# Kernel tuning notes

Hardware: AMD Instinct MI355X
Metric: run time of the kernel (lower is better)

The kernel has to match this reference:

```python
import jax, jax.numpy as jnp
import numpy as np
from jax import lax

S = 2048      # seq_len
E = 512       # loc_emb_size
H = 512       # hidden_size
V = 50000     # loc_size
WIN = 11      # window: j in [i-10, i]
LAMBDA_T = 0.1
LAMBDA_S = 50.0
DAY = 86400.0


def setup_inputs() -> dict:
    key = jax.random.key(0)
    ks = jax.random.split(key, 10)
    loc = jax.random.randint(ks[0], (S, 1), 0, V)
    # monotonically increasing timestamps spanning ~1 week
    tim = jnp.sort(jax.random.uniform(ks[1], (S,), dtype=jnp.float32) * (7.0 * DAY))
    coord = jax.random.uniform(ks[2], (S, 2), dtype=jnp.float32)
    emb = jax.random.normal(ks[3], (V, E), dtype=jnp.float32) * 0.02
    s_e = 1.0 / np.sqrt(E)
    s_h = 1.0 / np.sqrt(H)
    W_ih = jax.random.normal(ks[4], (3 * H, E), dtype=jnp.float32) * s_e
    W_hh = jax.random.normal(ks[5], (3 * H, H), dtype=jnp.float32) * s_h
    b_ih = jnp.zeros((3 * H,), dtype=jnp.float32)
    b_hh = jnp.zeros((3 * H,), dtype=jnp.float32)
    fc_w = jax.random.normal(ks[6], (V, H), dtype=jnp.float32) * s_h
    fc_b = jnp.zeros((V,), dtype=jnp.float32)
    return {"loc": loc, "tim": tim, "coord": coord, "emb": emb,
            "W_ih": W_ih, "W_hh": W_hh, "b_ih": b_ih, "b_hh": b_hh,
            "fc_w": fc_w, "fc_b": fc_b}


def _gru(x, W_ih, W_hh, b_ih, b_hh):
    # x: [S, E] -> out: [S, H]; PyTorch GRU equations (batch=1, 1 layer)
    xg = x @ W_ih.T + b_ih  # [S, 3H] precomputed input gates
    h0 = jnp.zeros((H,), dtype=x.dtype)

    def step(h, xg_t):
        hg = h @ W_hh.T + b_hh
        xr, xz, xn = jnp.split(xg_t, 3)
        hr, hz, hn = jnp.split(hg, 3)
        r = jax.nn.sigmoid(xr + hr)
        z = jax.nn.sigmoid(xz + hz)
        n = jnp.tanh(xn + r * hn)
        h_new = (1.0 - z) * n + z * h
        return h_new, h_new

    _, out = lax.scan(step, h0, xg)
    return out


def _flashback_core(out, tim, coord):
    # windowed spatiotemporal-decay weighted aggregation, fully vectorized
    i = jnp.arange(S)
    d = jnp.arange(WIN)                      # offsets 0..10
    j = i[:, None] - d[None, :]
    valid = j >= 0
    jc = jnp.maximum(j, 0)
    dt = tim[:, None] - tim[jc]
    diff = coord[:, None, :] - coord[jc]
    sq = jnp.sum(diff * diff, axis=-1)
    ds = jnp.sqrt(jnp.where(sq > 0, sq, 1.0)) * (sq > 0)  # safe norm (grad 0 at 0)
    f_t = (jnp.cos(dt * (2.0 * np.pi / DAY)) + 1.0) * 0.5 * jnp.exp(-(dt / DAY) * LAMBDA_T)
    f_s = jnp.exp(-ds * LAMBDA_S)
    w = jnp.where(valid, f_t * f_s + 1e-10, 0.0)
    out_w = jnp.einsum('sw,swh->sh', w, out[jc]) / jnp.sum(w, axis=1, keepdims=True)
    return out_w


def reference(loc, tim, coord, emb, W_ih, W_hh, b_ih, b_hh, fc_w, fc_b):
    x = emb[loc[:, 0]]                       # [S, E] (dropout is identity in eval)
    out = _gru(x, W_ih, W_hh, b_ih, b_hh)    # [S, H]
    out_w = _flashback_core(out, tim, coord) # [S, H]
    h = jax.nn.selu(out_w)
    y = h @ fc_w.T + fc_b                    # [S, V]
    return jax.nn.log_softmax(y, axis=-1)
```

## Files before the change

### kernel.cpp

```cpp
#include <hip/hip_runtime.h>
#include <math.h>

#define S_DIM 2048
#define H_DIM 512
#define V_DIM 50000
#define K_DIM 512
#define WINN 11
#define GRU_G 32

typedef __attribute__((ext_vector_type(4))) float f32x4;
typedef __attribute__((ext_vector_type(8))) __bf16 bf16x8;
typedef __attribute__((ext_vector_type(4))) unsigned int u32x4;

__device__ __forceinline__ unsigned int f2bf(float f) {
  union { float f; unsigned int u; } v; v.f = f;
  return (v.u + 0x7fffu + ((v.u >> 16) & 1u)) >> 16;
}
__device__ __forceinline__ unsigned int pack2(float a, float b) {
  return f2bf(a) | (f2bf(b) << 16);
}
__device__ __forceinline__ unsigned long long ld_pair(const unsigned long long* p) {
  return __hip_atomic_load(p, __ATOMIC_RELAXED, __HIP_MEMORY_SCOPE_AGENT);
}

__global__ void k_zero(int* p, int n) {
  int i = blockIdx.x * 256 + threadIdx.x;
  if (i < n) p[i] = 0;
}

__global__ void k_swizzle(const float* __restrict__ src, unsigned short* __restrict__ dst,
                          int rows_valid, int nchunks) {
  int c = blockIdx.x * 256 + threadIdx.x;
  if (c >= nchunks) return;
  int vt  = c >> 13;
  int m   = (c >> 6) & 127;
  int ktq = c & 63;
  int v = vt * 128 + m;
  f32x4 a = {0, 0, 0, 0}, b = {0, 0, 0, 0};
  if (v < rows_valid) {
    const float* s = src + (size_t)v * K_DIM + ktq * 8;
    a = *(const f32x4*)s;
    b = *(const f32x4*)(s + 4);
  }
  u32x4 pk;
  pk.x = pack2(a.x, a.y); pk.y = pack2(a.z, a.w);
  pk.z = pack2(b.x, b.y); pk.w = pack2(b.z, b.w);
  int kt = ktq >> 2, q = ktq & 3;
  int cd = vt * 8192 + kt * 512 + q * 128 + m;
  *(u32x4*)(dst + (size_t)cd * 8) = pk;
}

__global__ void k_gather(const float* __restrict__ emb, const int* __restrict__ loc,
                         unsigned short* __restrict__ dst) {
  int c = blockIdx.x * 256 + threadIdx.x;
  int st  = c >> 13;
  int m   = (c >> 6) & 127;
  int ktq = c & 63;
  int s = st * 128 + m;
  int l = loc[s];
  const float* sp = emb + (size_t)l * K_DIM + ktq * 8;
  f32x4 a = *(const f32x4*)sp;
  f32x4 b = *(const f32x4*)(sp + 4);
  u32x4 pk;
  pk.x = pack2(a.x, a.y); pk.y = pack2(a.z, a.w);
  pk.z = pack2(b.x, b.y); pk.w = pack2(b.z, b.w);
  int kt = ktq >> 2, q = ktq & 3;
  int cd = st * 8192 + kt * 512 + q * 128 + m;
  *(u32x4*)(dst + (size_t)cd * 8) = pk;
}

__global__ __launch_bounds__(256) void k_gemm(const unsigned short* __restrict__ A,
                                              const unsigned short* __restrict__ B,
                                              const float* __restrict__ bias,
                                              float* __restrict__ C, int ldc, int nvalid,
                                              float* lse_acc) {
  __shared__ __align__(16) unsigned short Als[4096];
  __shared__ __align__(16) unsigned short Bls[4096];
  int t = threadIdx.x;
  int ntile = blockIdx.x, mtile = blockIdx.y;
  const unsigned short* Ab = A + (size_t)mtile * 65536;
  const unsigned short* Bb = B + (size_t)ntile * 65536;
  int wid = t >> 6, lane = t & 63;
  int qm = wid >> 1, qn = wid & 1;
  int l15 = lane & 15, q4 = lane >> 4;
  f32x4 acc[4][4];
#pragma unroll
  for (int i = 0; i < 4; i++)
#pragma unroll
    for (int j = 0; j < 4; j++) acc[i][j] = (f32x4){0, 0, 0, 0};

  for (int kt = 0; kt < 16; ++kt) {
    __syncthreads();
    ((u32x4*)Als)[t]       = ((const u32x4*)(Ab + kt * 4096))[t];
    ((u32x4*)Als)[t + 256] = ((const u32x4*)(Ab + kt * 4096))[t + 256];
    ((u32x4*)Bls)[t]       = ((const u32x4*)(Bb + kt * 4096))[t];
    ((u32x4*)Bls)[t + 256] = ((const u32x4*)(Bb + kt * 4096))[t + 256];
    __syncthreads();
    bf16x8 af[4], bfr[4];
#pragma unroll
    for (int i = 0; i < 4; i++)
      af[i] = *(const bf16x8*)(&Als[(q4 * 128 + qm * 64 + i * 16 + l15) * 8]);
#pragma unroll
    for (int j = 0; j < 4; j++)
      bfr[j] = *(const bf16x8*)(&Bls[(q4 * 128 + qn * 64 + j * 16 + l15) * 8]);
#pragma unroll
    for (int i = 0; i < 4; i++)
#pragma unroll
      for (int j = 0; j < 4; j++)
        acc[i][j] = __builtin_amdgcn_mfma_f32_16x16x32_bf16(af[i], bfr[j], acc[i][j], 0, 0, 0);
  }

  int m0 = mtile * 128 + qm * 64;
  int n0 = ntile * 128 + qn * 64;
  float bv[4];
#pragma unroll
  for (int j = 0; j < 4; j++) {
    int n = n0 + j * 16 + l15;
    bv[j] = (n < nvalid) ? bias[n] : 0.f;
  }
#pragma unroll
  for (int i = 0; i < 4; i++) {
#pragma unroll
    for (int e = 0; e < 4; e++) {
      int r = m0 + i * 16 + q4 * 4 + e;
      float rs = 0.f;
#pragma unroll
      for (int j = 0; j < 4; j++) {
        int n = n0 + j * 16 + l15;
        if (n < nvalid) {
          float y = acc[i][j][e] + bv[j];
          C[(size_t)r * ldc + n] = y;
          rs += expf(y);
        }
      }
      if (lse_acc) {
        rs += __shfl_xor(rs, 1, 64);
        rs += __shfl_xor(rs, 2, 64);
        rs += __shfl_xor(rs, 4, 64);
        rs += __shfl_xor(rs, 8, 64);
        if (l15 == 0) atomicAdd(&lse_acc[r], rs);
      }
    }
  }
}

__global__ __launch_bounds__(512, 1) void k_gru(const float* __restrict__ W_hh,
                                                const float* __restrict__ b_hh,
                                                const float* __restrict__ xg,
                                                unsigned long long* h_pairs,
                                                float* __restrict__ out_gru) {
  __shared__ __align__(16) float h_lds[2][512];
  int g = blockIdx.x;
  int t = threadIdx.x;
  int wv = t >> 6;
  int lane = t & 63;
  int cl = lane >> 5;
  int rem = lane & 31;
  int gate = rem >> 3;
  int kq = rem & 7;
  bool act = (gate < 3);
  int col = g * 16 + wv * 2 + cl;
  f32x4 wr[16];
  float bhh = 0.f;
  if (act) {
    int grow = gate * 512 + col;
    const float* wsrc = W_hh + (size_t)grow * K_DIM + kq * 64;
#pragma unroll
    for (int c = 0; c < 16; c++) wr[c] = *(const f32x4*)(wsrc + c * 4);
    bhh = b_hh[grow];
  }
  bool pub = (rem == 0);
  float ho = 0.f;
  int wj = t >> 2;
  int wp = ((wj ^ ((wj >> 4) & 7)) << 2) | (t & 3);

  for (int s = 0; s < S_DIM; ++s) {
    float xr = 0.f, xz = 0.f, xn = 0.f;
    if (pub) {
      const float* xrow = xg + (size_t)s * 1536;
      xr = xrow[col]; xz = xrow[512 + col]; xn = xrow[1024 + col];
    }

    unsigned long long* p = h_pairs + (size_t)(s & 1) * 512 + t;
    unsigned long long u = ld_pair(p);
    while ((unsigned)(u >> 32) != (unsigned)s) u = ld_pair(p);
    union { unsigned uu; float ff; } cv; cv.uu = (unsigned)u;
    float* hb = h_lds[s & 1];
    hb[wp] = cv.ff;
    __syncthreads();

    float a = 0.f;
    if (act) {
      const f32x4* h4 = (const f32x4*)hb;
      float p0 = 0.f, p1 = 0.f, p2 = 0.f, p3 = 0.f;
#pragma unroll
      for (int c = 0; c < 16; c += 4) {
        f32x4 h0 = h4[(kq * 16 + c)     ^ kq];
        f32x4 h1 = h4[(kq * 16 + c + 1) ^ kq];
        f32x4 h2 = h4[(kq * 16 + c + 2) ^ kq];
        f32x4 h3 = h4[(kq * 16 + c + 3) ^ kq];
        p0 += wr[c].x * h0.x + wr[c].y * h0.y + wr[c].z * h0.z + wr[c].w * h0.w;
        p1 += wr[c + 1].x * h1.x + wr[c + 1].y * h1.y + wr[c + 1].z * h1.z + wr[c + 1].w * h1.w;
        p2 += wr[c + 2].x * h2.x + wr[c + 2].y * h2.y + wr[c + 2].z * h2.z + wr[c + 2].w * h2.w;
        p3 += wr[c + 3].x * h3.x + wr[c + 3].y * h3.y + wr[c + 3].z * h3.z + wr[c + 3].w * h3.w;
      }
      a = (p0 + p1) + (p2 + p3);
    }
    a += __shfl_xor(a, 1, 64);
    a += __shfl_xor(a, 2, 64);
    a += __shfl_xor(a, 4, 64);
    a += bhh;
    int base = cl << 5;
    float hr = __shfl(a, base,      64);
    float hz = __shfl(a, base + 8,  64);
    float hn = __shfl(a, base + 16, 64);
    if (pub) {
      float rg = 1.f / (1.f + expf(-(xr + hr)));
      float zg = 1.f / (1.f + expf(-(xz + hz)));
      float nn = tanhf(xn + rg * hn);
      float hnew = (1.f - zg) * nn + zg * ho;
      union { float f; unsigned u; } pv; pv.f = hnew;
      unsigned long long up = ((unsigned long long)(unsigned)(s + 1) << 32) |
                              (unsigned long long)pv.u;
      __hip_atomic_store(h_pairs + (size_t)((s + 1) & 1) * 512 + col, up,
                         __ATOMIC_RELAXED, __HIP_MEMORY_SCOPE_AGENT);
      out_gru[(size_t)s * H_DIM + col] = hnew;
      ho = hnew;
    }
  }
}

__global__ __launch_bounds__(256) void k_flash(const float* __restrict__ out_gru,
                                               const float* __restrict__ tim,
                                               const float* __restrict__ coord,
                                               unsigned short* __restrict__ hs_sw) {
  __shared__ float hsl[512];
  int s = blockIdx.x;
  int t = threadIdx.x;
  float w[WINN];
  float ts = tim[s];
  float cx = coord[s * 2], cy = coord[s * 2 + 1];
  float wsum = 0.f;
#pragma unroll
  for (int d = 0; d < WINN; ++d) {
    int j = s - d;
    float wd = 0.f;
    if (j >= 0) {
      float dt = ts - tim[j];
      float dx = cx - coord[j * 2], dy = cy - coord[j * 2 + 1];
      float sq = dx * dx + dy * dy;
      float ds = sq > 0.f ? sqrtf(sq) : 0.f;
      float ft = (cosf(dt * 7.2722052166430395e-05f) + 1.f) * 0.5f *
                 expf(dt * -1.1574074074074074e-06f);
      float fs = expf(-50.f * ds);
      wd = ft * fs + 1e-10f;
    }
    w[d] = wd;
    wsum += wd;
  }
  float inv = 1.f / wsum;
  for (int h = t; h < H_DIM; h += 256) {
    float a = 0.f;
#pragma unroll
    for (int d = 0; d < WINN; ++d) {
      int j = s - d;
      if (j >= 0) a += w[d] * out_gru[(size_t)j * H_DIM + h];
    }
    a *= inv;
    float o = a > 0.f ? 1.0507009873554805f * a
                      : 1.7580993408473766f * expm1f(a);
    hsl[h] = o;
  }
  __syncthreads();
  if (t < 64) {
    int kt = t >> 2, q = t & 3;
    const float* p = &hsl[t * 8];
    u32x4 pk;
    pk.x = pack2(p[0], p[1]); pk.y = pack2(p[2], p[3]);
    pk.z = pack2(p[4], p[5]); pk.w = pack2(p[6], p[7]);
    int st = s >> 7, m = s & 127;
    int cd = st * 8192 + kt * 512 + q * 128 + m;
    *(u32x4*)(hs_sw + (size_t)cd * 8) = pk;
  }
}

__global__ __launch_bounds__(256) void k_sub(float* __restrict__ Y,
                                             const float* __restrict__ lse) {
  int i = blockIdx.x * 256 + threadIdx.x;
  const int n4 = S_DIM * (V_DIM / 4);
  if (i >= n4) return;
  int row = (i * 4) / V_DIM;
  f32x4* Y4 = (f32x4*)Y;
  f32x4 v = Y4[i];
  float l = logf(lse[row]);
  v.x -= l; v.y -= l; v.z -= l; v.w -= l;
  Y4[i] = v;
}

extern "C" void kernel_launch(void* const* d_in, const int* in_sizes, int n_in,
                              void* d_out, int out_size, void* d_ws, size_t ws_size,
                              hipStream_t stream) {
  const int*   loc   = (const int*)d_in[0];
  const float* tim   = (const float*)d_in[1];
  const float* coord = (const float*)d_in[2];
  const float* emb   = (const float*)d_in[3];
  const float* W_ih  = (const float*)d_in[4];
  const float* W_hh  = (const float*)d_in[5];
  const float* b_ih  = (const float*)d_in[6];
  const float* b_hh  = (const float*)d_in[7];
  const float* fc_w  = (const float*)d_in[8];
  const float* fc_b  = (const float*)d_in[9];
  float* Y = (float*)d_out;

  char* w = (char*)d_ws;
  unsigned long long* h_pairs = (unsigned long long*)(w);
  float* lse     = (float*)(w + 8192);
  float* xg      = (float*)(w + 16384);
  float* out_gru = (float*)(w + 12599296);
  unsigned short* x_sw   = (unsigned short*)(w + 16793600);
  unsigned short* wih_sw = (unsigned short*)(w + 18890752);
  unsigned short* hs_sw  = (unsigned short*)(w + 20463616);
  unsigned short* fcw_sw = (unsigned short*)(w + 22560768);

  k_zero<<<16, 256, 0, stream>>>((int*)w, 4096);
  k_swizzle<<<12512, 256, 0, stream>>>(fc_w, fcw_sw, 50000, 391 * 8192);
  k_swizzle<<<384, 256, 0, stream>>>(W_ih, wih_sw, 1536, 12 * 8192);
  k_gather<<<512, 256, 0, stream>>>(emb, loc, x_sw);
  dim3 gx(12, 16);
  k_gemm<<<gx, 256, 0, stream>>>(x_sw, wih_sw, b_ih, xg, 1536, 1536, nullptr);
  k_gru<<<GRU_G, 512, 0, stream>>>(W_hh, b_hh, xg, h_pairs, out_gru);
  k_flash<<<2048, 256, 0, stream>>>(out_gru, tim, coord, hs_sw);
  dim3 gy(391, 16);
  k_gemm<<<gy, 256, 0, stream>>>(hs_sw, fcw_sw, fc_b, Y, 50000, 50000, lse);
  k_sub<<<100000, 256, 0, stream>>>(Y, lse);
}
```

Before: 5.915 ms.

## Restructure GRU recurrence block to 256 threads with 4 rows per lane group

The GRU step kernel now uses 256 threads per block instead of 512. Three waves each handle one gate, and each 16-lane group computes four output rows over a 32-element K slice, so every LDS read of h is reused across four weight rows. Partial sums are reduced with shuffles, staged through a small LDS array, and finished by 16 threads after an extra barrier. The gate math also switches to fast __expf and an exp-based tanh. The aim is to shorten the serial per-step latency of the recurrence, at the cost of a second barrier per step and slightly less accurate transcendentals.

Measured after the change: 4.899 ms. 17.2% less time.

```diff
diff --git a/kernel.cpp b/kernel.cpp
--- a/kernel.cpp
+++ b/kernel.cpp
@@ -144,80 +144,90 @@
   }
 }
 
-__global__ __launch_bounds__(512, 1) void k_gru(const float* __restrict__ W_hh,
+__global__ __launch_bounds__(256, 1) void k_gru(const float* __restrict__ W_hh,
                                                 const float* __restrict__ b_hh,
                                                 const float* __restrict__ xg,
                                                 unsigned long long* h_pairs,
                                                 float* __restrict__ out_gru) {
   __shared__ __align__(16) float h_lds[2][512];
-  int g = blockIdx.x;
+  __shared__ float hg_l[48];
+  int wg = blockIdx.x;
   int t = threadIdx.x;
   int wv = t >> 6;
   int lane = t & 63;
-  int cl = lane >> 5;
-  int rem = lane & 31;
-  int gate = rem >> 3;
-  int kq = rem & 7;
-  bool act = (gate < 3);
-  int col = g * 16 + wv * 2 + cl;
-  f32x4 wr[16];
-  float bhh = 0.f;
+  int cg = lane >> 4;
+  int kq = lane & 15;
+  bool act = (wv < 3);
+  f32x4 wr[4][8];
+  float bhh[4];
   if (act) {
-    int grow = gate * 512 + col;
-    const float* wsrc = W_hh + (size_t)grow * K_DIM + kq * 64;
-#pragma unroll
-    for (int c = 0; c < 16; c++) wr[c] = *(const f32x4*)(wsrc + c * 4);
-    bhh = b_hh[grow];
-  }
-  bool pub = (rem == 0);
+#pragma unroll
+    for (int c = 0; c < 4; c++) {
+      int grow = wv * 512 + wg * 16 + cg * 4 + c;
+      const float* wsrc = W_hh + (size_t)grow * K_DIM + kq * 32;
+#pragma unroll
+      for (int v = 0; v < 8; v++) wr[c][v] = *(const f32x4*)(wsrc + v * 4);
+      bhh[c] = b_hh[grow];
+    }
+  }
+  int col = wg * 16 + t;
   float ho = 0.f;
-  int wj = t >> 2;
-  int wp = ((wj ^ ((wj >> 4) & 7)) << 2) | (t & 3);
+  int j0 = t >> 2;
+  int wp0 = ((j0 ^ ((j0 >> 3) & 7)) << 2) | (t & 3);
+  int j1 = (t + 256) >> 2;
+  int wp1 = ((j1 ^ ((j1 >> 3) & 7)) << 2) | (t & 3);
 
   for (int s = 0; s < S_DIM; ++s) {
     float xr = 0.f, xz = 0.f, xn = 0.f;
-    if (pub) {
+    if (t < 16) {
       const float* xrow = xg + (size_t)s * 1536;
       xr = xrow[col]; xz = xrow[512 + col]; xn = xrow[1024 + col];
     }
 
-    unsigned long long* p = h_pairs + (size_t)(s & 1) * 512 + t;
-    unsigned long long u = ld_pair(p);
-    while ((unsigned)(u >> 32) != (unsigned)s) u = ld_pair(p);
-    union { unsigned uu; float ff; } cv; cv.uu = (unsigned)u;
+    unsigned long long* p0 = h_pairs + (size_t)(s & 1) * 512 + t;
+    unsigned long long* p1 = p0 + 256;
+    unsigned long long u0 = ld_pair(p0), u1 = ld_pair(p1);
+    while ((unsigned)(u0 >> 32) != (unsigned)s) u0 = ld_pair(p0);
+    while ((unsigned)(u1 >> 32) != (unsigned)s) u1 = ld_pair(p1);
+    union { unsigned u; float f; } c0, c1;
+    c0.u = (unsigned)u0; c1.u = (unsigned)u1;
     float* hb = h_lds[s & 1];
-    hb[wp] = cv.ff;
+    hb[wp0] = c0.f;
+    hb[wp1] = c1.f;
     __syncthreads();
 
-    float a = 0.f;
+    float pr[4] = {0.f, 0.f, 0.f, 0.f};
     if (act) {
       const f32x4* h4 = (const f32x4*)hb;
-      float p0 = 0.f, p1 = 0.f, p2 = 0.f, p3 = 0.f;
-#pragma unroll
-      for (int c = 0; c < 16; c += 4) {
-        f32x4 h0 = h4[(kq * 16 + c)     ^ kq];
-        f32x4 h1 = h4[(kq * 16 + c + 1) ^ kq];
-        f32x4 h2 = h4[(kq * 16 + c + 2) ^ kq];
-        f32x4 h3 = h4[(kq * 16 + c + 3) ^ kq];
-        p0 += wr[c].x * h0.x + wr[c].y * h0.y + wr[c].z * h0.z + wr[c].w * h0.w;
-        p1 += wr[c + 1].x * h1.x + wr[c + 1].y * h1.y + wr[c + 1].z * h1.z + wr[c + 1].w * h1.w;
-        p2 += wr[c + 2].x * h2.x + wr[c + 2].y * h2.y + wr[c + 2].z * h2.z + wr[c + 2].w * h2.w;
-        p3 += wr[c + 3].x * h3.x + wr[c + 3].y * h3.y + wr[c + 3].z * h3.z + wr[c + 3].w * h3.w;
+#pragma unroll
+      for (int v = 0; v < 8; v++) {
+        f32x4 hv = h4[(kq * 8 + v) ^ (kq & 7)];
+#pragma unroll
+        for (int c = 0; c < 4; c++) {
+          pr[c] += wr[c][v].x * hv.x + wr[c][v].y * hv.y +
+                   wr[c][v].z * hv.z + wr[c][v].w * hv.w;
+        }
       }
-      a = (p0 + p1) + (p2 + p3);
-    }
-    a += __shfl_xor(a, 1, 64);
-    a += __shfl_xor(a, 2, 64);
-    a += __shfl_xor(a, 4, 64);
-    a += bhh;
-    int base = cl << 5;
-    float hr = __shfl(a, base,      64);
-    float hz = __shfl(a, base + 8,  64);
-    float hn = __shfl(a, base + 16, 64);
-    if (pub) {
-      float rg = 1.f / (1.f + expf(-(xr + hr)));
-      float zg = 1.f / (1.f + expf(-(xz + hz)));
-      float nn = tanhf(xn + rg * hn);
+    }
+#pragma unroll
+    for (int c = 0; c < 4; c++) {
+      pr[c] += __shfl_xor(pr[c], 1, 64);
+      pr[c] += __shfl_xor(pr[c], 2, 64);
+      pr[c] += __shfl_xor(pr[c], 4, 64);
+      pr[c] += __shfl_xor(pr[c], 8, 64);
+    }
+    if (act && kq == 0) {
+#pragma unroll
+      for (int c = 0; c < 4; c++) hg_l[wv * 16 + cg * 4 + c] = pr[c] + bhh[c];
+    }
+    __syncthreads();
+
+    if (t < 16) {
+      float hr = hg_l[t], hz = hg_l[16 + t], hn = hg_l[32 + t];
+      float rg = 1.f / (1.f + __expf(-(xr + hr)));
+      float zg = 1.f / (1.f + __expf(-(xz + hz)));
+      float e2 = __expf(2.f * (xn + rg * hn));
+      float nn = 1.f - 2.f / (e2 + 1.f);
       float hnew = (1.f - zg) * nn + zg * ho;
       union { float f; unsigned u; } pv; pv.f = hnew;
       unsigned long long up = ((unsigned long long)(unsigned)(s + 1) << 32) |
@@ -328,7 +338,7 @@
   k_gather<<<512, 256, 0, stream>>>(emb, loc, x_sw);
   dim3 gx(12, 16);
   k_gemm<<<gx, 256, 0, stream>>>(x_sw, wih_sw, b_ih, xg, 1536, 1536, nullptr);
-  k_gru<<<GRU_G, 512, 0, stream>>>(W_hh, b_hh, xg, h_pairs, out_gru);
+  k_gru<<<GRU_G, 256, 0, stream>>>(W_hh, b_hh, xg, h_pairs, out_gru);
   k_flash<<<2048, 256, 0, stream>>>(out_gru, tim, coord, hs_sw);
   dim3 gy(391, 16);
   k_gemm<<<gy, 256, 0, stream>>>(hs_sw, fcw_sw, fc_b, Y, 50000, 50000, lse);
```
